# Performance work log

Hardware: AMD Instinct MI355X
Metric: run time of the kernel (lower is better)

Reference implementation:

```python
import jax, jax.numpy as jnp
import numpy as np

N = 100000   # nodes
E = 1200000  # edges
D = 64       # in_channels == out_channels, heads=1
NEG_SLOPE = 0.2  # PyG GATv2Conv default negative_slope


def setup_inputs() -> dict:
    key = jax.random.key(0)
    k1, k2, k3, k4 = jax.random.split(key, 4)
    x = jax.random.normal(k1, (N, D), dtype=jnp.float32)
    edge_index = jax.random.randint(k2, (2, E), 0, N, dtype=jnp.int32)
    # glorot-ish scale for shared linear (share_weights=True -> lin_l == lin_r)
    W = jax.random.normal(k3, (D, D), dtype=jnp.float32) * (1.0 / np.sqrt(D))
    b = jnp.zeros((D,), dtype=jnp.float32)
    att = jax.random.normal(k4, (D,), dtype=jnp.float32) * (1.0 / np.sqrt(D))
    return {"x": x, "edge_index": edge_index, "W": W, "b": b, "att": att}


def reference(x, edge_index, W, b, att):
    src = edge_index[0]  # source j (messages flow j -> i)
    dst = edge_index[1]  # target i
    # shared linear transform (share_weights=True)
    z = x @ W.T + b                                   # [N, D]
    # GATv2 score: att . leakyrelu(z_j + z_i)
    e = jax.nn.leaky_relu(z[src] + z[dst], NEG_SLOPE) @ att  # [E]
    # segment softmax over incoming edges of each target node
    m = jax.ops.segment_max(e, dst, num_segments=N)   # [N]
    ex = jnp.exp(e - m[dst])                          # [E]
    s = jax.ops.segment_sum(ex, dst, num_segments=N)  # [N]
    alpha = ex / s[dst]                               # [E]
    # SimpleConv(aggr='sum') with edge_weight=alpha on ORIGINAL x
    out = jax.ops.segment_sum(alpha[:, None] * x[src], dst, num_segments=N)  # [N, D]
    return out
```

## Files before the change

kernel.cpp:

```cpp
#include <hip/hip_runtime.h>

#define D 64
#define LOG2E 1.4426950408889634f

__device__ __forceinline__ unsigned short f2bf(float f) {
    unsigned int bits = __float_as_uint(f);
    return (unsigned short)((bits + 0x7fffu + ((bits >> 16) & 1u)) >> 16);
}

__global__ __launch_bounds__(256) void gemm_z_count(const float* __restrict__ x,
                                                    const float* __restrict__ W,
                                                    const float* __restrict__ b,
                                                    unsigned int* __restrict__ zxb,
                                                    int n,
                                                    const int* __restrict__ dst,
                                                    int* __restrict__ deg,
                                                    int* __restrict__ slot,
                                                    int e_cnt) {
    __shared__ float wt[D * 65];
    __shared__ float xs[64 * D];
    int tid = threadIdx.x;

    int gtid = blockIdx.x * 256 + tid;
    int nthreads = gridDim.x * 256;
    int e0 = -1, e1 = -1, e2 = -1, s0 = 0, s1 = 0, s2 = 0;
    {
        int ee = gtid;
        if (ee < e_cnt) { e0 = ee; s0 = atomicAdd(&deg[dst[ee]], 1); ee += nthreads; }
        if (ee < e_cnt) { e1 = ee; s1 = atomicAdd(&deg[dst[ee]], 1); ee += nthreads; }
        if (ee < e_cnt) { e2 = ee; s2 = atomicAdd(&deg[dst[ee]], 1); }
    }

    for (int i = tid; i < D * D; i += 256) {
        int j = i >> 6, k = i & 63;
        wt[k * 65 + j] = W[i];
    }
    int row0 = blockIdx.x * 64;
    for (int i = tid; i < 64 * D / 4; i += 256) {
        int r = row0 + (i >> 4);
        float4 v = (r < n) ? ((const float4*)x)[(size_t)r * 16 + (i & 15)]
                           : make_float4(0.f, 0.f, 0.f, 0.f);
        ((float4*)xs)[i] = v;
    }
    __syncthreads();
    int col = tid & 63;
    int w   = tid >> 6;
    float bb = b[col];
    float acc[16];
#pragma unroll
    for (int r = 0; r < 16; ++r) acc[r] = bb;

    for (int k4 = 0; k4 < D; k4 += 4) {
        float wv0 = wt[(k4 + 0) * 65 + col];
        float wv1 = wt[(k4 + 1) * 65 + col];
        float wv2 = wt[(k4 + 2) * 65 + col];
        float wv3 = wt[(k4 + 3) * 65 + col];
#pragma unroll
        for (int r = 0; r < 16; ++r) {
            const float4 xv = *(const float4*)&xs[(w * 16 + r) * D + k4];
            acc[r] += xv.x * wv0 + xv.y * wv1 + xv.z * wv2 + xv.w * wv3;
        }
    }
#pragma unroll
    for (int r = 0; r < 16; ++r) {
        int row = row0 + w * 16 + r;
        if (row < n) {
            float xv = xs[(w * 16 + r) * D + col];
            unsigned int u = (unsigned int)f2bf(acc[r]) |
                             ((unsigned int)f2bf(xv) << 16);
            zxb[(size_t)row * 64 + col] = u;
        }
    }

    if (e0 >= 0) slot[e0] = s0;
    if (e1 >= 0) slot[e1] = s1;
    if (e2 >= 0) slot[e2] = s2;
}

__global__ __launch_bounds__(256) void scan_part(const int* __restrict__ deg,
                                                 int* __restrict__ part, int n) {
    __shared__ int red[256];
    int t = threadIdx.x;
    int i = blockIdx.x * 256 + t;
    red[t] = (i < n) ? deg[i] : 0;
    __syncthreads();
    for (int off = 128; off >= 1; off >>= 1) {
        if (t < off) red[t] += red[t + off];
        __syncthreads();
    }
    if (t == 0) part[blockIdx.x] = red[0];
}

__global__ __launch_bounds__(512) void scan_top(int* __restrict__ part, int B) {
    __shared__ int s[512];
    int t = threadIdx.x;
    int v = (t < B) ? part[t] : 0;
    s[t] = v;
    __syncthreads();
    for (int off = 1; off < 512; off <<= 1) {
        int u = (t >= off) ? s[t - off] : 0;
        __syncthreads();
        s[t] += u;
        __syncthreads();
    }
    if (t < B) part[t] = s[t] - v;
}

__global__ __launch_bounds__(256) void scan_final(const int* __restrict__ deg,
                                                  const int* __restrict__ part,
                                                  int* __restrict__ rowstart, int n) {
    __shared__ int s[256];
    int t = threadIdx.x;
    int i = blockIdx.x * 256 + t;
    int v = (i < n) ? deg[i] : 0;
    s[t] = v;
    __syncthreads();
    for (int off = 1; off < 256; off <<= 1) {
        int u = (t >= off) ? s[t - off] : 0;
        __syncthreads();
        s[t] += u;
        __syncthreads();
    }
    int incl = s[t] + part[blockIdx.x];
    if (i < n) rowstart[i] = incl - v;
    if (i == n - 1) rowstart[n] = incl;
}

__global__ __launch_bounds__(256) void csr_fill_slot(const int* __restrict__ src,
                                                     const int* __restrict__ dst,
                                                     const int* __restrict__ rowstart,
                                                     const int* __restrict__ slot,
                                                     int* __restrict__ srcids, int e_cnt) {
    int e = blockIdx.x * 256 + threadIdx.x;
    if (e >= e_cnt) return;
    srcids[rowstart[dst[e]] + slot[e]] = src[e];
}

__global__ __launch_bounds__(256) void gather4b(const int* __restrict__ srcids,
                                                const int* __restrict__ rowstart,
                                                const unsigned int* __restrict__ zxb,
                                                const float* __restrict__ att,
                                                float* __restrict__ out, int n) {
    int lane = threadIdx.x & 63;
    int node = blockIdx.x * 4 + (threadIdx.x >> 6);
    if (node >= n) return;
    int q = lane & 15;
    int h = lane >> 4;
    int rs = rowstart[node], re = rowstart[node + 1];

    const uint4 zdv = *(const uint4*)(zxb + (size_t)node * 64 + 4 * q);
    float zd0 = __uint_as_float(zdv.x << 16);
    float zd1 = __uint_as_float(zdv.y << 16);
    float zd2 = __uint_as_float(zdv.z << 16);
    float zd3 = __uint_as_float(zdv.w << 16);
    float4 av = *(const float4*)(att + 4 * q);
    float a0 = av.x * LOG2E, a1 = av.y * LOG2E, a2 = av.z * LOG2E, a3 = av.w * LOG2E;

    float ax0 = 0.f, ax1 = 0.f, ax2 = 0.f, ax3 = 0.f, ssum = 0.f;
    for (int e = rs; e < re; e += 8) {
        int e0i = e + h, e1i = e + 4 + h;
        bool l0 = e0i < re, l1 = e1i < re;
        int s0 = l0 ? srcids[e0i] : node;
        int s1 = l1 ? srcids[e1i] : node;
        const uint4 r0 = *(const uint4*)(zxb + (size_t)s0 * 64 + 4 * q);
        const uint4 r1 = *(const uint4*)(zxb + (size_t)s1 * 64 + 4 * q);

        float v0 = __uint_as_float(r0.x << 16) + zd0; v0 = v0 > 0.f ? v0 : 0.2f * v0;
        float v1 = __uint_as_float(r0.y << 16) + zd1; v1 = v1 > 0.f ? v1 : 0.2f * v1;
        float v2 = __uint_as_float(r0.z << 16) + zd2; v2 = v2 > 0.f ? v2 : 0.2f * v2;
        float v3 = __uint_as_float(r0.w << 16) + zd3; v3 = v3 > 0.f ? v3 : 0.2f * v3;
        float p0 = v0 * a0 + v1 * a1 + v2 * a2 + v3 * a3;

        float u0 = __uint_as_float(r1.x << 16) + zd0; u0 = u0 > 0.f ? u0 : 0.2f * u0;
        float u1 = __uint_as_float(r1.y << 16) + zd1; u1 = u1 > 0.f ? u1 : 0.2f * u1;
        float u2 = __uint_as_float(r1.z << 16) + zd2; u2 = u2 > 0.f ? u2 : 0.2f * u2;
        float u3 = __uint_as_float(r1.w << 16) + zd3; u3 = u3 > 0.f ? u3 : 0.2f * u3;
        float p1 = u0 * a0 + u1 * a1 + u2 * a2 + u3 * a3;

#pragma unroll
        for (int off = 8; off >= 1; off >>= 1) {
            p0 += __shfl_xor(p0, off, 64);
            p1 += __shfl_xor(p1, off, 64);
        }
        float ex0 = l0 ? __builtin_exp2f(p0) : 0.f;
        float ex1 = l1 ? __builtin_exp2f(p1) : 0.f;
        ssum += ex0 + ex1;
        ax0 += ex0 * __uint_as_float(r0.x & 0xffff0000u)
             + ex1 * __uint_as_float(r1.x & 0xffff0000u);
        ax1 += ex0 * __uint_as_float(r0.y & 0xffff0000u)
             + ex1 * __uint_as_float(r1.y & 0xffff0000u);
        ax2 += ex0 * __uint_as_float(r0.z & 0xffff0000u)
             + ex1 * __uint_as_float(r1.z & 0xffff0000u);
        ax3 += ex0 * __uint_as_float(r0.w & 0xffff0000u)
             + ex1 * __uint_as_float(r1.w & 0xffff0000u);
    }
    ssum += __shfl_xor(ssum, 16, 64); ssum += __shfl_xor(ssum, 32, 64);
    ax0  += __shfl_xor(ax0, 16, 64);  ax0  += __shfl_xor(ax0, 32, 64);
    ax1  += __shfl_xor(ax1, 16, 64);  ax1  += __shfl_xor(ax1, 32, 64);
    ax2  += __shfl_xor(ax2, 16, 64);  ax2  += __shfl_xor(ax2, 32, 64);
    ax3  += __shfl_xor(ax3, 16, 64);  ax3  += __shfl_xor(ax3, 32, 64);
    if (h == 0) {
        float inv = (re > rs) ? 1.f / ssum : 0.f;
        float4 o = make_float4(ax0 * inv, ax1 * inv, ax2 * inv, ax3 * inv);
        *(float4*)&out[(size_t)node * D + 4 * q] = o;
    }
}

extern "C" void kernel_launch(void* const* d_in, const int* in_sizes, int n_in,
                              void* d_out, int out_size, void* d_ws, size_t ws_size,
                              hipStream_t stream) {
    const float* x   = (const float*)d_in[0];
    const int*   ei  = (const int*)d_in[1];
    const float* W   = (const float*)d_in[2];
    const float* b   = (const float*)d_in[3];
    const float* att = (const float*)d_in[4];
    int n = in_sizes[0] / D;
    int e = in_sizes[1] / 2;
    const int* src = ei;
    const int* dst = ei + e;
    float* out = (float*)d_out;

    int nBlkN = (n + 255) / 256;
    int gemmBlk = (n + 63) / 64;

    unsigned int* zxb = (unsigned int*)d_ws;
    int* deg      = (int*)(zxb + (size_t)n * 64);
    int* rowstart = deg + n;
    int* srcids   = rowstart + n + 1;
    int* slot     = srcids + e;
    int* part     = slot + e;

    hipMemsetAsync(deg, 0, (size_t)n * sizeof(int), stream);
    gemm_z_count<<<gemmBlk, 256, 0, stream>>>(x, W, b, zxb, n, dst, deg, slot, e);
    scan_part<<<nBlkN, 256, 0, stream>>>(deg, part, n);
    scan_top<<<1, 512, 0, stream>>>(part, nBlkN);
    scan_final<<<nBlkN, 256, 0, stream>>>(deg, part, rowstart, n);
    csr_fill_slot<<<(e + 255) / 256, 256, 0, stream>>>(src, dst, rowstart, slot, srcids, e);
    gather4b<<<(n + 3) / 4, 256, 0, stream>>>(srcids, rowstart, zxb, att, out, n);
}
```

Before: 233.1 us.

## Use fp16 packed math in gather, partition degree counters and CSR fill

```diff
diff --git a/kernel.cpp b/kernel.cpp
--- a/kernel.cpp
+++ b/kernel.cpp
@@ -2,10 +2,27 @@
 
 #define D 64
 #define LOG2E 1.4426950408889634f
-
-__device__ __forceinline__ unsigned short f2bf(float f) {
-    unsigned int bits = __float_as_uint(f);
-    return (unsigned short)((bits + 0x7fffu + ((bits >> 16) & 1u)) >> 16);
+#define NPART 8
+
+typedef _Float16 hv2 __attribute__((ext_vector_type(2)));
+
+__device__ __forceinline__ hv2 u2h(unsigned int u) { return __builtin_bit_cast(hv2, u); }
+__device__ __forceinline__ unsigned int h2u(hv2 h) { return __builtin_bit_cast(unsigned int, h); }
+
+__device__ __forceinline__ float fdot2f(hv2 a, hv2 b, float c) {
+#if __has_builtin(__builtin_amdgcn_fdot2)
+    return __builtin_amdgcn_fdot2(a, b, c, false);
+#else
+    return c + (float)a.x * (float)b.x + (float)a.y * (float)b.y;
+#endif
+}
+
+__device__ __forceinline__ hv2 lrelu2(hv2 v) {
+    hv2 m = v * (_Float16)0.2f;
+    hv2 r;
+    r.x = v.x > (_Float16)0.f ? v.x : m.x;
+    r.y = v.y > (_Float16)0.f ? v.y : m.y;
+    return r;
 }
 
 __global__ __launch_bounds__(256) void gemm_z_count(const float* __restrict__ x,
@@ -14,7 +31,7 @@
                                                     unsigned int* __restrict__ zxb,
                                                     int n,
                                                     const int* __restrict__ dst,
-                                                    int* __restrict__ deg,
+                                                    int* __restrict__ deg8,
                                                     int* __restrict__ slot,
                                                     int e_cnt) {
     __shared__ float wt[D * 65];
@@ -23,12 +40,13 @@
 
     int gtid = blockIdx.x * 256 + tid;
     int nthreads = gridDim.x * 256;
+    int* mydeg = deg8 + (size_t)(blockIdx.x & (NPART - 1)) * n;
     int e0 = -1, e1 = -1, e2 = -1, s0 = 0, s1 = 0, s2 = 0;
     {
         int ee = gtid;
-        if (ee < e_cnt) { e0 = ee; s0 = atomicAdd(&deg[dst[ee]], 1); ee += nthreads; }
-        if (ee < e_cnt) { e1 = ee; s1 = atomicAdd(&deg[dst[ee]], 1); ee += nthreads; }
-        if (ee < e_cnt) { e2 = ee; s2 = atomicAdd(&deg[dst[ee]], 1); }
+        if (ee < e_cnt) { e0 = ee; s0 = atomicAdd(&mydeg[dst[ee]], 1); ee += nthreads; }
+        if (ee < e_cnt) { e1 = ee; s1 = atomicAdd(&mydeg[dst[ee]], 1); ee += nthreads; }
+        if (ee < e_cnt) { e2 = ee; s2 = atomicAdd(&mydeg[dst[ee]], 1); }
     }
 
     for (int i = tid; i < D * D; i += 256) {
@@ -61,14 +79,21 @@
             acc[r] += xv.x * wv0 + xv.y * wv1 + xv.z * wv2 + xv.w * wv3;
         }
     }
+    bool odd = col & 1;
 #pragma unroll
     for (int r = 0; r < 16; ++r) {
         int row = row0 + w * 16 + r;
+        float z = acc[r];
+        float xv = xs[(w * 16 + r) * D + col];
+        float zsh = __shfl_xor(z, 1, 64);
+        float xsh = __shfl_xor(xv, 1, 64);
+        float lo = odd ? xsh : z;
+        float hi = odd ? xv : zsh;
         if (row < n) {
-            float xv = xs[(w * 16 + r) * D + col];
-            unsigned int u = (unsigned int)f2bf(acc[r]) |
-                             ((unsigned int)f2bf(xv) << 16);
-            zxb[(size_t)row * 64 + col] = u;
+            hv2 hp;
+            hp.x = (_Float16)lo;
+            hp.y = (_Float16)hi;
+            zxb[(size_t)row * 64 + col] = h2u(hp);
         }
     }
 
@@ -77,12 +102,16 @@
     if (e2 >= 0) slot[e2] = s2;
 }
 
-__global__ __launch_bounds__(256) void scan_part(const int* __restrict__ deg,
-                                                 int* __restrict__ part, int n) {
+__global__ __launch_bounds__(256) void scan_part8(const int* __restrict__ deg8,
+                                                  int* __restrict__ part, int n) {
     __shared__ int red[256];
     int t = threadIdx.x;
     int i = blockIdx.x * 256 + t;
-    red[t] = (i < n) ? deg[i] : 0;
+    int s = 0;
+    if (i < n)
+#pragma unroll
+        for (int c = 0; c < NPART; ++c) s += deg8[(size_t)c * n + i];
+    red[t] = s;
     __syncthreads();
     for (int off = 128; off >= 1; off >>= 1) {
         if (t < off) red[t] += red[t + off];
@@ -106,14 +135,18 @@
     if (t < B) part[t] = s[t] - v;
 }
 
-__global__ __launch_bounds__(256) void scan_final(const int* __restrict__ deg,
-                                                  const int* __restrict__ part,
-                                                  int* __restrict__ rowstart, int n) {
+__global__ __launch_bounds__(256) void scan_final8(int* __restrict__ deg8,
+                                                   const int* __restrict__ part,
+                                                   int* __restrict__ rowstart, int n) {
     __shared__ int s[256];
     int t = threadIdx.x;
     int i = blockIdx.x * 256 + t;
-    int v = (i < n) ? deg[i] : 0;
-    s[t] = v;
+    int dc[NPART];
+    int tot = 0;
+    if (i < n)
+#pragma unroll
+        for (int c = 0; c < NPART; ++c) { dc[c] = deg8[(size_t)c * n + i]; tot += dc[c]; }
+    s[t] = tot;
     __syncthreads();
     for (int off = 1; off < 256; off <<= 1) {
         int u = (t >= off) ? s[t - off] : 0;
@@ -122,21 +155,37 @@
         __syncthreads();
     }
     int incl = s[t] + part[blockIdx.x];
-    if (i < n) rowstart[i] = incl - v;
+    if (i < n) {
+        int run = incl - tot;
+        rowstart[i] = run;
+#pragma unroll
+        for (int c = 0; c < NPART; ++c) { int tmp = dc[c]; deg8[(size_t)c * n + i] = run; run += tmp; }
+    }
     if (i == n - 1) rowstart[n] = incl;
 }
 
-__global__ __launch_bounds__(256) void csr_fill_slot(const int* __restrict__ src,
+__global__ __launch_bounds__(256) void csr_fill_part(const int* __restrict__ src,
                                                      const int* __restrict__ dst,
-                                                     const int* __restrict__ rowstart,
+                                                     const int* __restrict__ base8,
                                                      const int* __restrict__ slot,
-                                                     int* __restrict__ srcids, int e_cnt) {
-    int e = blockIdx.x * 256 + threadIdx.x;
-    if (e >= e_cnt) return;
-    srcids[rowstart[dst[e]] + slot[e]] = src[e];
-}
-
-__global__ __launch_bounds__(256) void gather4b(const int* __restrict__ srcids,
+                                                     int* __restrict__ srcids,
+                                                     int e_cnt, int n, int T) {
+    int g  = blockIdx.x & (NPART - 1);
+    int gb = blockIdx.x >> 3;
+    int gstride = (gridDim.x >> 3) * 256;
+    int nper = (n + NPART - 1) / NPART;
+    int lo = g * nper, hi = min(lo + nper, n);
+    for (int e = gb * 256 + threadIdx.x; e < e_cnt; e += gstride) {
+        int d = dst[e];
+        if (d < lo || d >= hi) continue;
+        int em = e;
+        while (em >= T) em -= T;
+        int c = (em >> 8) & (NPART - 1);
+        srcids[base8[(size_t)c * n + d] + slot[e]] = src[e];
+    }
+}
+
+__global__ __launch_bounds__(256) void gather4h(const int* __restrict__ srcids,
                                                 const int* __restrict__ rowstart,
                                                 const unsigned int* __restrict__ zxb,
                                                 const float* __restrict__ att,
@@ -149,14 +198,14 @@
     int rs = rowstart[node], re = rowstart[node + 1];
 
     const uint4 zdv = *(const uint4*)(zxb + (size_t)node * 64 + 4 * q);
-    float zd0 = __uint_as_float(zdv.x << 16);
-    float zd1 = __uint_as_float(zdv.y << 16);
-    float zd2 = __uint_as_float(zdv.z << 16);
-    float zd3 = __uint_as_float(zdv.w << 16);
+    hv2 zd01 = u2h(zdv.x), zd23 = u2h(zdv.z);
     float4 av = *(const float4*)(att + 4 * q);
-    float a0 = av.x * LOG2E, a1 = av.y * LOG2E, a2 = av.z * LOG2E, a3 = av.w * LOG2E;
-
-    float ax0 = 0.f, ax1 = 0.f, ax2 = 0.f, ax3 = 0.f, ssum = 0.f;
+    hv2 at01, at23;
+    at01.x = (_Float16)av.x; at01.y = (_Float16)av.y;
+    at23.x = (_Float16)av.z; at23.y = (_Float16)av.w;
+
+    hv2 ax01 = (hv2)(_Float16)0.f, ax23 = (hv2)(_Float16)0.f;
+    float ssum = 0.f;
     for (int e = rs; e < re; e += 8) {
         int e0i = e + h, e1i = e + 4 + h;
         bool l0 = e0i < re, l1 = e1i < re;
@@ -165,43 +214,38 @@
         const uint4 r0 = *(const uint4*)(zxb + (size_t)s0 * 64 + 4 * q);
         const uint4 r1 = *(const uint4*)(zxb + (size_t)s1 * 64 + 4 * q);
 
-        float v0 = __uint_as_float(r0.x << 16) + zd0; v0 = v0 > 0.f ? v0 : 0.2f * v0;
-        float v1 = __uint_as_float(r0.y << 16) + zd1; v1 = v1 > 0.f ? v1 : 0.2f * v1;
-        float v2 = __uint_as_float(r0.z << 16) + zd2; v2 = v2 > 0.f ? v2 : 0.2f * v2;
-        float v3 = __uint_as_float(r0.w << 16) + zd3; v3 = v3 > 0.f ? v3 : 0.2f * v3;
-        float p0 = v0 * a0 + v1 * a1 + v2 * a2 + v3 * a3;
-
-        float u0 = __uint_as_float(r1.x << 16) + zd0; u0 = u0 > 0.f ? u0 : 0.2f * u0;
-        float u1 = __uint_as_float(r1.y << 16) + zd1; u1 = u1 > 0.f ? u1 : 0.2f * u1;
-        float u2 = __uint_as_float(r1.z << 16) + zd2; u2 = u2 > 0.f ? u2 : 0.2f * u2;
-        float u3 = __uint_as_float(r1.w << 16) + zd3; u3 = u3 > 0.f ? u3 : 0.2f * u3;
-        float p1 = u0 * a0 + u1 * a1 + u2 * a2 + u3 * a3;
+        hv2 v01 = lrelu2(u2h(r0.x) + zd01);
+        hv2 v23 = lrelu2(u2h(r0.z) + zd23);
+        float p0 = fdot2f(v23, at23, fdot2f(v01, at01, 0.f));
+
+        hv2 w01 = lrelu2(u2h(r1.x) + zd01);
+        hv2 w23 = lrelu2(u2h(r1.z) + zd23);
+        float p1 = fdot2f(w23, at23, fdot2f(w01, at01, 0.f));
 
 #pragma unroll
         for (int off = 8; off >= 1; off >>= 1) {
             p0 += __shfl_xor(p0, off, 64);
             p1 += __shfl_xor(p1, off, 64);
         }
-        float ex0 = l0 ? __builtin_exp2f(p0) : 0.f;
-        float ex1 = l1 ? __builtin_exp2f(p1) : 0.f;
+        float ex0 = l0 ? __builtin_exp2f(p0 * LOG2E) : 0.f;
+        float ex1 = l1 ? __builtin_exp2f(p1 * LOG2E) : 0.f;
         ssum += ex0 + ex1;
-        ax0 += ex0 * __uint_as_float(r0.x & 0xffff0000u)
-             + ex1 * __uint_as_float(r1.x & 0xffff0000u);
-        ax1 += ex0 * __uint_as_float(r0.y & 0xffff0000u)
-             + ex1 * __uint_as_float(r1.y & 0xffff0000u);
-        ax2 += ex0 * __uint_as_float(r0.z & 0xffff0000u)
-             + ex1 * __uint_as_float(r1.z & 0xffff0000u);
-        ax3 += ex0 * __uint_as_float(r0.w & 0xffff0000u)
-             + ex1 * __uint_as_float(r1.w & 0xffff0000u);
+        hv2 e0h; e0h.x = (_Float16)ex0; e0h.y = (_Float16)ex0;
+        hv2 e1h; e1h.x = (_Float16)ex1; e1h.y = (_Float16)ex1;
+        ax01 = e0h * u2h(r0.y) + ax01;
+        ax23 = e0h * u2h(r0.w) + ax23;
+        ax01 = e1h * u2h(r1.y) + ax01;
+        ax23 = e1h * u2h(r1.w) + ax23;
     }
     ssum += __shfl_xor(ssum, 16, 64); ssum += __shfl_xor(ssum, 32, 64);
-    ax0  += __shfl_xor(ax0, 16, 64);  ax0  += __shfl_xor(ax0, 32, 64);
-    ax1  += __shfl_xor(ax1, 16, 64);  ax1  += __shfl_xor(ax1, 32, 64);
-    ax2  += __shfl_xor(ax2, 16, 64);  ax2  += __shfl_xor(ax2, 32, 64);
-    ax3  += __shfl_xor(ax3, 16, 64);  ax3  += __shfl_xor(ax3, 32, 64);
+    ax01 = ax01 + u2h(__shfl_xor(h2u(ax01), 16, 64));
+    ax01 = ax01 + u2h(__shfl_xor(h2u(ax01), 32, 64));
+    ax23 = ax23 + u2h(__shfl_xor(h2u(ax23), 16, 64));
+    ax23 = ax23 + u2h(__shfl_xor(h2u(ax23), 32, 64));
     if (h == 0) {
         float inv = (re > rs) ? 1.f / ssum : 0.f;
-        float4 o = make_float4(ax0 * inv, ax1 * inv, ax2 * inv, ax3 * inv);
+        float4 o = make_float4((float)ax01.x * inv, (float)ax01.y * inv,
+                               (float)ax23.x * inv, (float)ax23.y * inv);
         *(float4*)&out[(size_t)node * D + 4 * q] = o;
     }
 }
@@ -220,21 +264,22 @@
     const int* dst = ei + e;
     float* out = (float*)d_out;
 
-    int nBlkN = (n + 255) / 256;
+    int nBlkN   = (n + 255) / 256;
     int gemmBlk = (n + 63) / 64;
+    int T       = gemmBlk * 256;
 
     unsigned int* zxb = (unsigned int*)d_ws;
-    int* deg      = (int*)(zxb + (size_t)n * 64);
-    int* rowstart = deg + n;
+    int* deg8     = (int*)(zxb + (size_t)n * 64);
+    int* rowstart = deg8 + (size_t)NPART * n;
     int* srcids   = rowstart + n + 1;
     int* slot     = srcids + e;
     int* part     = slot + e;
 
-    hipMemsetAsync(deg, 0, (size_t)n * sizeof(int), stream);
-    gemm_z_count<<<gemmBlk, 256, 0, stream>>>(x, W, b, zxb, n, dst, deg, slot, e);
-    scan_part<<<nBlkN, 256, 0, stream>>>(deg, part, n);
+    (void)hipMemsetAsync(deg8, 0, (size_t)NPART * n * sizeof(int), stream);
+    gemm_z_count<<<gemmBlk, 256, 0, stream>>>(x, W, b, zxb, n, dst, deg8, slot, e);
+    scan_part8<<<nBlkN, 256, 0, stream>>>(deg8, part, n);
     scan_top<<<1, 512, 0, stream>>>(part, nBlkN);
-    scan_final<<<nBlkN, 256, 0, stream>>>(deg, part, rowstart, n);
-    csr_fill_slot<<<(e + 255) / 256, 256, 0, stream>>>(src, dst, rowstart, slot, srcids, e);
-    gather4b<<<(n + 3) / 4, 256, 0, stream>>>(srcids, rowstart, zxb, att, out, n);
-}
+    scan_final8<<<nBlkN, 256, 0, stream>>>(deg8, part, rowstart, n);
+    csr_fill_part<<<1024, 256, 0, stream>>>(src, dst, deg8, slot, srcids, e, n, T);
+    gather4h<<<(n + 3) / 4, 256, 0, stream>>>(srcids, rowstart, zxb, att, out, n);
+}
```

Result: slower. 244.2 us (+4.8%).
